# Optimization experiments

Measured on AMD Instinct MI355X. Metric: run time of the kernel, lower is better.

The kernel has to match this reference:

```python
import jax, jax.numpy as jnp
import numpy as np

B, T, D, H, E, K = 4, 1024, 1024, 2048, 8, 2  # batch, tokens, model_dim, ffn hidden, experts, top-k


def setup_inputs() -> dict:
    key = jax.random.key(0)
    k0, k1, k2, k3 = jax.random.split(key, 4)
    return {
        "x": jax.random.normal(k0, (B, T, D), dtype=jnp.float32),
        "wg": jax.random.normal(k1, (D, E), dtype=jnp.float32) * 0.02,   # gate projection
        "w1": jax.random.normal(k2, (E, D, H), dtype=jnp.float32) * 0.02,  # expert fc1
        "b1": jnp.zeros((E, H), dtype=jnp.float32),
        "w2": jax.random.normal(k3, (E, H, D), dtype=jnp.float32) * 0.02,  # expert fc2
        "b2": jnp.zeros((E, D), dtype=jnp.float32),
    }


def _moe(x, wg, w1, b1, w2, b2):
    N = B * T
    xt = x.reshape(N, D)
    # --- gating: softmax scores, top-2 selection, normalize selected gates ---
    logits = xt @ wg                         # [N, E]
    scores = jax.nn.softmax(logits, axis=-1)
    vals, idx = jax.lax.top_k(scores, K)     # [N, K]
    vals = vals / jnp.sum(vals, axis=-1, keepdims=True)
    # combine weights: [N, E], nonzero only at the top-k experts per token
    combine = jnp.zeros((N, E), dtype=xt.dtype).at[
        jnp.arange(N)[:, None], idx
    ].add(vals)
    # --- expert FFN (activation_fn is identity per source) ---
    h = jnp.einsum('nd,edh->neh', xt, w1) + b1   # [N, E, H]
    o = jnp.einsum('neh,ehd->ned', h, w2) + b2   # [N, E, D]
    # --- combine / scatter back ---
    y = jnp.einsum('ne,ned->nd', combine, o)     # [N, D]
    return y.reshape(B, T, D)


def reference(x, wg, w1, b1, w2, b2):
    y = _moe(x, wg, w1, b1, w2, b2)              # [B, T, D]
    s = jnp.sum(y, axis=2)                       # [B, T]
    return jax.nn.log_softmax(s, axis=1)
```

## Files before the change

### kernel.cpp

```cpp
#include <hip/hip_runtime.h>
#include <stdint.h>

#define B_ 4
#define T_ 1024
#define D_ 1024
#define H_ 2048
#define E_ 8

__device__ __forceinline__ void stage16(const float* g, float* l) {
    __builtin_amdgcn_global_load_lds(
        (const __attribute__((address_space(1))) uint32_t*)g,
        (__attribute__((address_space(3))) uint32_t*)l, 16, 0, 0);
}

__global__ __launch_bounds__(256) void w2sum_kernel(const float* __restrict__ w2,
                                                    float* __restrict__ w2sum) {
    __shared__ float buf[3][4 * D_];
    const int wid = threadIdx.x >> 6, lane = threadIdx.x & 63;
    const float* src = w2 + (size_t)blockIdx.x * 32 * D_ + wid * D_ + lane * 4;

#define A_STAGE(k)                                                        \
    {                                                                     \
        const float* s_ = src + (k) * (4 * D_);                           \
        float* d_ = &buf[(k) % 3][wid * D_];                              \
        stage16(s_,       d_);       stage16(s_ + 256, d_ + 256);         \
        stage16(s_ + 512, d_ + 512); stage16(s_ + 768, d_ + 768);         \
    }

    A_STAGE(0); A_STAGE(1);
    float accs[8];
#pragma unroll
    for (int k = 0; k < 8; ++k) {
        if (k < 7) asm volatile("s_waitcnt vmcnt(4)" ::: "memory");
        else       asm volatile("s_waitcnt vmcnt(0)" ::: "memory");
        if (k < 6) A_STAGE(k + 2);
        const float* row = &buf[k % 3][wid * D_];
        float acc = 0.f;
#pragma unroll
        for (int j = 0; j < 4; ++j) {
            float4 a = *(const float4*)&row[j * 256 + lane * 4];
            acc += a.x + a.y + a.z + a.w;
        }
#pragma unroll
        for (int off = 32; off >= 1; off >>= 1) acc += __shfl_xor(acc, off, 64);
        accs[k] = acc;
    }
    if (lane == 0) {
        int r0 = blockIdx.x * 32 + wid;
#pragma unroll
        for (int k = 0; k < 8; ++k) w2sum[r0 + k * 4] = accs[k];
    }
#undef A_STAGE
}

__global__ __launch_bounds__(256) void v_build_kernel(const float* __restrict__ w1,
                                                      const float* __restrict__ w2sum,
                                                      const float* __restrict__ b1,
                                                      const float* __restrict__ b2,
                                                      float* __restrict__ vT,
                                                      float* __restrict__ c) {
    __shared__ float buf[2][4 * H_];
    const int bid = blockIdx.x;
    const int e   = bid >> 6;
    const int d0  = (bid & 63) * 16;
    const int wid = threadIdx.x >> 6, lane = threadIdx.x & 63;
    const float* src = w1 + ((size_t)e * D_ + d0 + wid) * H_ + lane * 4;

    const float4* wsp = (const float4*)(w2sum + (size_t)e * H_) + lane;
    float4 s0 = wsp[0],   s1 = wsp[64],  s2 = wsp[128], s3 = wsp[192],
           s4 = wsp[256], s5 = wsp[320], s6 = wsp[384], s7 = wsp[448];
    asm volatile("" ::: "memory");

#define B_STAGE(k)                                                         \
    {                                                                      \
        const float* s_ = src + (size_t)(k) * 4 * H_;                      \
        float* d_ = &buf[(k) & 1][wid * H_];                               \
        stage16(s_,        d_);        stage16(s_ + 256,  d_ + 256);       \
        stage16(s_ + 512,  d_ + 512);  stage16(s_ + 768,  d_ + 768);       \
        stage16(s_ + 1024, d_ + 1024); stage16(s_ + 1280, d_ + 1280);      \
        stage16(s_ + 1536, d_ + 1536); stage16(s_ + 1792, d_ + 1792);      \
    }

    B_STAGE(0); B_STAGE(1);
    float accs[4];
#pragma unroll
    for (int k = 0; k < 4; ++k) {
        if (k < 3) asm volatile("s_waitcnt vmcnt(8)" ::: "memory");
        else       asm volatile("s_waitcnt vmcnt(0)" ::: "memory");
        const float* row = &buf[k & 1][wid * H_];
        float acc;
        {
            float4 a0 = *(const float4*)&row[0 * 256 + lane * 4];
            float4 a1 = *(const float4*)&row[1 * 256 + lane * 4];
            float4 a2 = *(const float4*)&row[2 * 256 + lane * 4];
            float4 a3 = *(const float4*)&row[3 * 256 + lane * 4];
            float4 a4 = *(const float4*)&row[4 * 256 + lane * 4];
            float4 a5 = *(const float4*)&row[5 * 256 + lane * 4];
            float4 a6 = *(const float4*)&row[6 * 256 + lane * 4];
            float4 a7 = *(const float4*)&row[7 * 256 + lane * 4];
            acc = a0.x*s0.x + a0.y*s0.y + a0.z*s0.z + a0.w*s0.w
                + a1.x*s1.x + a1.y*s1.y + a1.z*s1.z + a1.w*s1.w
                + a2.x*s2.x + a2.y*s2.y + a2.z*s2.z + a2.w*s2.w
                + a3.x*s3.x + a3.y*s3.y + a3.z*s3.z + a3.w*s3.w
                + a4.x*s4.x + a4.y*s4.y + a4.z*s4.z + a4.w*s4.w
                + a5.x*s5.x + a5.y*s5.y + a5.z*s5.z + a5.w*s5.w
                + a6.x*s6.x + a6.y*s6.y + a6.z*s6.z + a6.w*s6.w
                + a7.x*s7.x + a7.y*s7.y + a7.z*s7.z + a7.w*s7.w;
        }
#pragma unroll
        for (int off = 32; off >= 1; off >>= 1) acc += __shfl_xor(acc, off, 64);
        accs[k] = acc;
        if (k < 2) B_STAGE(k + 2);
    }
    if (lane == 0) {
#pragma unroll
        for (int k = 0; k < 4; ++k)
            vT[(size_t)(d0 + k * 4 + wid) * E_ + e] = accs[k];
    }

    if ((bid & 63) == 0 && wid == 0) {
        const float4* bp = (const float4*)(b1 + (size_t)e * H_) + lane;
        float4 q0 = bp[0],   q1 = bp[64],  q2 = bp[128], q3 = bp[192],
               q4 = bp[256], q5 = bp[320], q6 = bp[384], q7 = bp[448];
        float s = q0.x*s0.x + q0.y*s0.y + q0.z*s0.z + q0.w*s0.w
                + q1.x*s1.x + q1.y*s1.y + q1.z*s1.z + q1.w*s1.w
                + q2.x*s2.x + q2.y*s2.y + q2.z*s2.z + q2.w*s2.w
                + q3.x*s3.x + q3.y*s3.y + q3.z*s3.z + q3.w*s3.w
                + q4.x*s4.x + q4.y*s4.y + q4.z*s4.z + q4.w*s4.w
                + q5.x*s5.x + q5.y*s5.y + q5.z*s5.z + q5.w*s5.w
                + q6.x*s6.x + q6.y*s6.y + q6.z*s6.z + q6.w*s6.w
                + q7.x*s7.x + q7.y*s7.y + q7.z*s7.z + q7.w*s7.w;
        const float4* cp = (const float4*)(b2 + (size_t)e * D_) + lane;
#pragma unroll
        for (int j = 0; j < 4; ++j) {
            float4 bb = cp[j * 64];
            s += bb.x + bb.y + bb.z + bb.w;
        }
#pragma unroll
        for (int off = 32; off >= 1; off >>= 1) s += __shfl_xor(s, off, 64);
        if (lane == 0) c[e] = s;
    }
#undef B_STAGE
}

__global__ __launch_bounds__(256) void token_kernel(const float* __restrict__ x,
                                                    const float* __restrict__ wg,
                                                    const float* __restrict__ vT,
                                                    const float* __restrict__ c,
                                                    float* __restrict__ s) {
    int wid  = threadIdx.x >> 6;
    int lane = threadIdx.x & 63;
    int n = blockIdx.x * 4 + wid;
    const float* xr = x + (size_t)n * D_;

    float lg[E_] = {0.f,0.f,0.f,0.f,0.f,0.f,0.f,0.f};
    float dv[E_] = {0.f,0.f,0.f,0.f,0.f,0.f,0.f,0.f};

#pragma unroll
    for (int k = 0; k < D_ / 64; ++k) {
        int d = lane + 64 * k;
        float xv = xr[d];
        const float4* wgp = (const float4*)(wg + (size_t)d * E_);
        const float4* vp  = (const float4*)(vT + (size_t)d * E_);
        float4 g0 = wgp[0], g1 = wgp[1];
        float4 v0 = vp[0],  v1 = vp[1];
        lg[0] += xv * g0.x; lg[1] += xv * g0.y; lg[2] += xv * g0.z; lg[3] += xv * g0.w;
        lg[4] += xv * g1.x; lg[5] += xv * g1.y; lg[6] += xv * g1.z; lg[7] += xv * g1.w;
        dv[0] += xv * v0.x; dv[1] += xv * v0.y; dv[2] += xv * v0.z; dv[3] += xv * v0.w;
        dv[4] += xv * v1.x; dv[5] += xv * v1.y; dv[6] += xv * v1.z; dv[7] += xv * v1.w;
    }

#pragma unroll
    for (int off = 32; off >= 1; off >>= 1) {
#pragma unroll
        for (int e = 0; e < E_; ++e) {
            lg[e] += __shfl_xor(lg[e], off, 64);
            dv[e] += __shfl_xor(dv[e], off, 64);
        }
    }

    if (lane == 0) {
        int e0 = 0;
#pragma unroll
        for (int e = 1; e < E_; ++e) if (lg[e] > lg[e0]) e0 = e;
        int e1 = (e0 == 0) ? 1 : 0;
#pragma unroll
        for (int e = 0; e < E_; ++e) {
            if (e == e0) continue;
            if (lg[e] > lg[e1]) e1 = e;
        }
        float l0 = lg[e0], l1 = lg[e1];
        float g1w = 1.f / (1.f + expf(l0 - l1));
        float g0w = 1.f - g1w;
        s[n] = g0w * (dv[e0] + c[e0]) + g1w * (dv[e1] + c[e1]);
    }
}

__global__ __launch_bounds__(64) void lsm_kernel(const float* __restrict__ s,
                                                 float* __restrict__ out) {
    int brow = blockIdx.x;
    int lane = threadIdx.x & 63;
    const float* row = s + (size_t)brow * T_;
    float vals[16];
    float mx = -3.0e38f;
#pragma unroll
    for (int k = 0; k < 16; ++k) {
        vals[k] = row[lane + 64 * k];
        mx = fmaxf(mx, vals[k]);
    }
#pragma unroll
    for (int off = 32; off >= 1; off >>= 1) mx = fmaxf(mx, __shfl_xor(mx, off, 64));
    float sm = 0.f;
#pragma unroll
    for (int k = 0; k < 16; ++k) sm += expf(vals[k] - mx);
#pragma unroll
    for (int off = 32; off >= 1; off >>= 1) sm += __shfl_xor(sm, off, 64);
    float lse = mx + logf(sm);
#pragma unroll
    for (int k = 0; k < 16; ++k) out[(size_t)brow * T_ + lane + 64 * k] = vals[k] - lse;
}

extern "C" void kernel_launch(void* const* d_in, const int* in_sizes, int n_in,
                              void* d_out, int out_size, void* d_ws, size_t ws_size,
                              hipStream_t stream) {
    const float* x  = (const float*)d_in[0];
    const float* wg = (const float*)d_in[1];
    const float* w1 = (const float*)d_in[2];
    const float* b1 = (const float*)d_in[3];
    const float* w2 = (const float*)d_in[4];
    const float* b2 = (const float*)d_in[5];
    float* out = (float*)d_out;

    float* ws     = (float*)d_ws;
    float* w2sum  = ws;
    float* vT     = ws + 16384;
    float* c      = ws + 24576;
    float* s      = ws + 24592;

    w2sum_kernel<<<dim3(512), dim3(256), 0, stream>>>(w2, w2sum);
    v_build_kernel<<<dim3(512), dim3(256), 0, stream>>>(w1, w2sum, b1, b2, vT, c);
    token_kernel<<<dim3(1024), dim3(256), 0, stream>>>(x, wg, vT, c, s);
    lsm_kernel<<<dim3(4), dim3(64), 0, stream>>>(s, out);
}
```

Before: 45.12 us.

## Fuse token scoring and log-softmax via last-block atomic counter

New measurement: 58.53 us. +29.7%, slower.

```diff
diff --git a/kernel.cpp b/kernel.cpp
--- a/kernel.cpp
+++ b/kernel.cpp
@@ -7,50 +7,66 @@
 #define H_ 2048
 #define E_ 8
 
+#define AL(p)    __hip_atomic_load((p), __ATOMIC_RELAXED, __HIP_MEMORY_SCOPE_AGENT)
+#define AS(p, v) __hip_atomic_store((p), (v), __ATOMIC_RELAXED, __HIP_MEMORY_SCOPE_AGENT)
+
 __device__ __forceinline__ void stage16(const float* g, float* l) {
     __builtin_amdgcn_global_load_lds(
         (const __attribute__((address_space(1))) uint32_t*)g,
         (__attribute__((address_space(3))) uint32_t*)l, 16, 0, 0);
 }
 
+__device__ __forceinline__ void load4x16_sc(const float* p0, const float* p1,
+                                            const float* p2, const float* p3,
+                                            float4& r0, float4& r1,
+                                            float4& r2, float4& r3) {
+    asm volatile(
+        "global_load_dwordx4 %0, %4, off sc0 sc1\n\t"
+        "global_load_dwordx4 %1, %5, off sc0 sc1\n\t"
+        "global_load_dwordx4 %2, %6, off sc0 sc1\n\t"
+        "global_load_dwordx4 %3, %7, off sc0 sc1\n\t"
+        "s_waitcnt vmcnt(0)"
+        : "=&v"(r0), "=&v"(r1), "=&v"(r2), "=&v"(r3)
+        : "v"(p0), "v"(p1), "v"(p2), "v"(p3)
+        : "memory");
+}
+
 __global__ __launch_bounds__(256) void w2sum_kernel(const float* __restrict__ w2,
                                                     float* __restrict__ w2sum) {
-    __shared__ float buf[3][4 * D_];
+    __shared__ float buf[3][4096];
     const int wid = threadIdx.x >> 6, lane = threadIdx.x & 63;
-    const float* src = w2 + (size_t)blockIdx.x * 32 * D_ + wid * D_ + lane * 4;
-
-#define A_STAGE(k)                                                        \
-    {                                                                     \
-        const float* s_ = src + (k) * (4 * D_);                           \
-        float* d_ = &buf[(k) % 3][wid * D_];                              \
-        stage16(s_,       d_);       stage16(s_ + 256, d_ + 256);         \
-        stage16(s_ + 512, d_ + 512); stage16(s_ + 768, d_ + 768);         \
-    }
-
-    A_STAGE(0); A_STAGE(1);
+    const float* src = w2 + ((size_t)blockIdx.x * 32 + wid) * D_ + lane * 4;
+
+#define ASTG(k) { const float* s_ = src + (size_t)(k) * 4 * D_;               \
+                  float* d_ = &buf[(k) % 3][wid * 1024];                      \
+                  stage16(s_, d_);         stage16(s_ + 256, d_ + 256);       \
+                  stage16(s_ + 512, d_ + 512); stage16(s_ + 768, d_ + 768); }
+    ASTG(0); ASTG(1);
     float accs[8];
 #pragma unroll
     for (int k = 0; k < 8; ++k) {
         if (k < 7) asm volatile("s_waitcnt vmcnt(4)" ::: "memory");
         else       asm volatile("s_waitcnt vmcnt(0)" ::: "memory");
-        if (k < 6) A_STAGE(k + 2);
-        const float* row = &buf[k % 3][wid * D_];
-        float acc = 0.f;
-#pragma unroll
-        for (int j = 0; j < 4; ++j) {
-            float4 a = *(const float4*)&row[j * 256 + lane * 4];
-            acc += a.x + a.y + a.z + a.w;
-        }
-#pragma unroll
-        for (int off = 32; off >= 1; off >>= 1) acc += __shfl_xor(acc, off, 64);
-        accs[k] = acc;
+        if (k < 6) ASTG(k + 2);
+        const float* row = &buf[k % 3][wid * 1024];
+        float4 a0 = *(const float4*)&row[0 * 256 + lane * 4];
+        float4 a1 = *(const float4*)&row[1 * 256 + lane * 4];
+        float4 a2 = *(const float4*)&row[2 * 256 + lane * 4];
+        float4 a3 = *(const float4*)&row[3 * 256 + lane * 4];
+        accs[k] = (a0.x + a0.y + a0.z + a0.w) + (a1.x + a1.y + a1.z + a1.w)
+                + (a2.x + a2.y + a2.z + a2.w) + (a3.x + a3.y + a3.z + a3.w);
+    }
+#undef ASTG
+#pragma unroll
+    for (int off = 32; off >= 1; off >>= 1) {
+#pragma unroll
+        for (int k = 0; k < 8; ++k) accs[k] += __shfl_xor(accs[k], off, 64);
     }
     if (lane == 0) {
-        int r0 = blockIdx.x * 32 + wid;
+        const int r0 = blockIdx.x * 32 + wid;
 #pragma unroll
         for (int k = 0; k < 8; ++k) w2sum[r0 + k * 4] = accs[k];
     }
-#undef A_STAGE
 }
 
 __global__ __launch_bounds__(256) void v_build_kernel(const float* __restrict__ w1,
@@ -71,7 +87,7 @@
            s4 = wsp[256], s5 = wsp[320], s6 = wsp[384], s7 = wsp[448];
     asm volatile("" ::: "memory");
 
-#define B_STAGE(k)                                                         \
+#define BSTG(k)                                                            \
     {                                                                      \
         const float* s_ = src + (size_t)(k) * 4 * H_;                      \
         float* d_ = &buf[(k) & 1][wid * H_];                               \
@@ -81,7 +97,7 @@
         stage16(s_ + 1536, d_ + 1536); stage16(s_ + 1792, d_ + 1792);      \
     }
 
-    B_STAGE(0); B_STAGE(1);
+    BSTG(0); BSTG(1);
     float accs[4];
 #pragma unroll
     for (int k = 0; k < 4; ++k) {
@@ -107,10 +123,14 @@
                 + a6.x*s6.x + a6.y*s6.y + a6.z*s6.z + a6.w*s6.w
                 + a7.x*s7.x + a7.y*s7.y + a7.z*s7.z + a7.w*s7.w;
         }
-#pragma unroll
-        for (int off = 32; off >= 1; off >>= 1) acc += __shfl_xor(acc, off, 64);
         accs[k] = acc;
-        if (k < 2) B_STAGE(k + 2);
+        if (k < 2) BSTG(k + 2);
+    }
+#undef BSTG
+#pragma unroll
+    for (int off = 32; off >= 1; off >>= 1) {
+#pragma unroll
+        for (int k = 0; k < 4; ++k) accs[k] += __shfl_xor(accs[k], off, 64);
     }
     if (lane == 0) {
 #pragma unroll
@@ -140,84 +160,120 @@
         for (int off = 32; off >= 1; off >>= 1) s += __shfl_xor(s, off, 64);
         if (lane == 0) c[e] = s;
     }
-#undef B_STAGE
-}
-
-__global__ __launch_bounds__(256) void token_kernel(const float* __restrict__ x,
-                                                    const float* __restrict__ wg,
-                                                    const float* __restrict__ vT,
-                                                    const float* __restrict__ c,
-                                                    float* __restrict__ s) {
-    int wid  = threadIdx.x >> 6;
-    int lane = threadIdx.x & 63;
-    int n = blockIdx.x * 4 + wid;
-    const float* xr = x + (size_t)n * D_;
-
-    float lg[E_] = {0.f,0.f,0.f,0.f,0.f,0.f,0.f,0.f};
-    float dv[E_] = {0.f,0.f,0.f,0.f,0.f,0.f,0.f,0.f};
-
-#pragma unroll
-    for (int k = 0; k < D_ / 64; ++k) {
-        int d = lane + 64 * k;
-        float xv = xr[d];
-        const float4* wgp = (const float4*)(wg + (size_t)d * E_);
-        const float4* vp  = (const float4*)(vT + (size_t)d * E_);
-        float4 g0 = wgp[0], g1 = wgp[1];
-        float4 v0 = vp[0],  v1 = vp[1];
-        lg[0] += xv * g0.x; lg[1] += xv * g0.y; lg[2] += xv * g0.z; lg[3] += xv * g0.w;
-        lg[4] += xv * g1.x; lg[5] += xv * g1.y; lg[6] += xv * g1.z; lg[7] += xv * g1.w;
-        dv[0] += xv * v0.x; dv[1] += xv * v0.y; dv[2] += xv * v0.z; dv[3] += xv * v0.w;
-        dv[4] += xv * v1.x; dv[5] += xv * v1.y; dv[6] += xv * v1.z; dv[7] += xv * v1.w;
+}
+
+__global__ __launch_bounds__(256) void cd_kernel(
+    const float* __restrict__ x,  const float* __restrict__ wg,
+    const float* __restrict__ vT, const float* __restrict__ cbuf,
+    float* __restrict__ sbuf, unsigned* __restrict__ ccnt,
+    float* __restrict__ out)
+{
+    const int wid  = threadIdx.x >> 6;
+    const int lane = threadIdx.x & 63;
+    const int n0   = (blockIdx.x * 4 + wid) * 2;
+    const float* x0 = x + (size_t)n0 * D_;
+    const float* x1 = x0 + D_;
+
+    float lgA[E_] = {0,0,0,0,0,0,0,0}, dvA[E_] = {0,0,0,0,0,0,0,0};
+    float lgB[E_] = {0,0,0,0,0,0,0,0}, dvB[E_] = {0,0,0,0,0,0,0,0};
+
+#pragma unroll
+    for (int it = 0; it < 4; ++it) {
+        const int dbase = it * 256 + lane * 4;
+        float4 xa4 = *(const float4*)&x0[dbase];
+        float4 xb4 = *(const float4*)&x1[dbase];
+#pragma unroll
+        for (int dd = 0; dd < 4; ++dd) {
+            float xa = (dd == 0) ? xa4.x : (dd == 1) ? xa4.y : (dd == 2) ? xa4.z : xa4.w;
+            float xb = (dd == 0) ? xb4.x : (dd == 1) ? xb4.y : (dd == 2) ? xb4.z : xb4.w;
+            const float4* wgp = (const float4*)(wg + (size_t)(dbase + dd) * E_);
+            const float4* vp  = (const float4*)(vT + (size_t)(dbase + dd) * E_);
+            float4 g0 = wgp[0], g1 = wgp[1];
+            float4 v0 = vp[0],  v1 = vp[1];
+            lgA[0] += xa * g0.x; lgA[1] += xa * g0.y; lgA[2] += xa * g0.z; lgA[3] += xa * g0.w;
+            lgA[4] += xa * g1.x; lgA[5] += xa * g1.y; lgA[6] += xa * g1.z; lgA[7] += xa * g1.w;
+            dvA[0] += xa * v0.x; dvA[1] += xa * v0.y; dvA[2] += xa * v0.z; dvA[3] += xa * v0.w;
+            dvA[4] += xa * v1.x; dvA[5] += xa * v1.y; dvA[6] += xa * v1.z; dvA[7] += xa * v1.w;
+            lgB[0] += xb * g0.x; lgB[1] += xb * g0.y; lgB[2] += xb * g0.z; lgB[3] += xb * g0.w;
+            lgB[4] += xb * g1.x; lgB[5] += xb * g1.y; lgB[6] += xb * g1.z; lgB[7] += xb * g1.w;
+            dvB[0] += xb * v0.x; dvB[1] += xb * v0.y; dvB[2] += xb * v0.z; dvB[3] += xb * v0.w;
+            dvB[4] += xb * v1.x; dvB[5] += xb * v1.y; dvB[6] += xb * v1.z; dvB[7] += xb * v1.w;
+        }
     }
 
 #pragma unroll
     for (int off = 32; off >= 1; off >>= 1) {
 #pragma unroll
-        for (int e = 0; e < E_; ++e) {
-            lg[e] += __shfl_xor(lg[e], off, 64);
-            dv[e] += __shfl_xor(dv[e], off, 64);
-        }
-    }
-
-    if (lane == 0) {
-        int e0 = 0;
-#pragma unroll
-        for (int e = 1; e < E_; ++e) if (lg[e] > lg[e0]) e0 = e;
-        int e1 = (e0 == 0) ? 1 : 0;
-#pragma unroll
-        for (int e = 0; e < E_; ++e) {
-            if (e == e0) continue;
-            if (lg[e] > lg[e1]) e1 = e;
-        }
-        float l0 = lg[e0], l1 = lg[e1];
-        float g1w = 1.f / (1.f + expf(l0 - l1));
-        float g0w = 1.f - g1w;
-        s[n] = g0w * (dv[e0] + c[e0]) + g1w * (dv[e1] + c[e1]);
-    }
-}
-
-__global__ __launch_bounds__(64) void lsm_kernel(const float* __restrict__ s,
-                                                 float* __restrict__ out) {
-    int brow = blockIdx.x;
-    int lane = threadIdx.x & 63;
-    const float* row = s + (size_t)brow * T_;
-    float vals[16];
-    float mx = -3.0e38f;
-#pragma unroll
-    for (int k = 0; k < 16; ++k) {
-        vals[k] = row[lane + 64 * k];
-        mx = fmaxf(mx, vals[k]);
-    }
-#pragma unroll
-    for (int off = 32; off >= 1; off >>= 1) mx = fmaxf(mx, __shfl_xor(mx, off, 64));
-    float sm = 0.f;
-#pragma unroll
-    for (int k = 0; k < 16; ++k) sm += expf(vals[k] - mx);
-#pragma unroll
-    for (int off = 32; off >= 1; off >>= 1) sm += __shfl_xor(sm, off, 64);
-    float lse = mx + logf(sm);
-#pragma unroll
-    for (int k = 0; k < 16; ++k) out[(size_t)brow * T_ + lane + 64 * k] = vals[k] - lse;
+        for (int q = 0; q < E_; ++q) {
+            lgA[q] += __shfl_xor(lgA[q], off, 64);
+            dvA[q] += __shfl_xor(dvA[q], off, 64);
+            lgB[q] += __shfl_xor(lgB[q], off, 64);
+            dvB[q] += __shfl_xor(dvB[q], off, 64);
+        }
+    }
+
+    if (lane == 0 || lane == 32) {
+        const bool isA = (lane == 0);
+        float lg[E_], dvr[E_];
+#pragma unroll
+        for (int q = 0; q < E_; ++q) {
+            lg[q]  = isA ? lgA[q] : lgB[q];
+            dvr[q] = isA ? dvA[q] : dvB[q];
+        }
+        float m0 = lg[0]; int i0 = 0;
+#pragma unroll
+        for (int q = 1; q < E_; ++q) if (lg[q] > m0) { m0 = lg[q]; i0 = q; }
+        float m1 = -3.0e38f; int i1 = 0;
+#pragma unroll
+        for (int q = 0; q < E_; ++q) if (q != i0 && lg[q] > m1) { m1 = lg[q]; i1 = q; }
+        float dv0 = 0.f, dv1 = 0.f, c0v = 0.f, c1v = 0.f;
+#pragma unroll
+        for (int q = 0; q < E_; ++q) {
+            if (q == i0) { dv0 += dvr[q]; c0v += cbuf[q]; }
+            if (q == i1) { dv1 += dvr[q]; c1v += cbuf[q]; }
+        }
+        float g1w = 1.f / (1.f + expf(m0 - m1));
+        AS(&sbuf[isA ? n0 : (n0 + 1)], (1.f - g1w) * (dv0 + c0v) + g1w * (dv1 + c1v));
+    }
+
+    asm volatile("s_waitcnt vmcnt(0)" ::: "memory");
+    __syncthreads();
+    __shared__ int islast;
+    if (threadIdx.x == 0) {
+        unsigned old = __hip_atomic_fetch_add(ccnt, 1u, __ATOMIC_RELAXED, __HIP_MEMORY_SCOPE_AGENT);
+        islast = (old == (unsigned)(gridDim.x - 1)) ? 1 : 0;
+    }
+    __syncthreads();
+    if (!islast) return;
+
+    {
+        const int brow = wid;
+        const float* row = sbuf + (size_t)brow * T_;
+        float4 v0, v1, v2, v3;
+        load4x16_sc(row + lane * 4 + 0 * 256, row + lane * 4 + 1 * 256,
+                    row + lane * 4 + 2 * 256, row + lane * 4 + 3 * 256,
+                    v0, v1, v2, v3);
+        float vals[16] = {v0.x, v0.y, v0.z, v0.w, v1.x, v1.y, v1.z, v1.w,
+                          v2.x, v2.y, v2.z, v2.w, v3.x, v3.y, v3.z, v3.w};
+        float mx = -3.0e38f;
+#pragma unroll
+        for (int k = 0; k < 16; ++k) mx = fmaxf(mx, vals[k]);
+#pragma unroll
+        for (int off = 32; off >= 1; off >>= 1) mx = fmaxf(mx, __shfl_xor(mx, off, 64));
+        float sm = 0.f;
+#pragma unroll
+        for (int k = 0; k < 16; ++k) sm += expf(vals[k] - mx);
+#pragma unroll
+        for (int off = 32; off >= 1; off >>= 1) sm += __shfl_xor(sm, off, 64);
+        float lse = mx + logf(sm);
+#pragma unroll
+        for (int j = 0; j < 4; ++j) {
+            float4 o;
+            o.x = vals[j * 4 + 0] - lse; o.y = vals[j * 4 + 1] - lse;
+            o.z = vals[j * 4 + 2] - lse; o.w = vals[j * 4 + 3] - lse;
+            *(float4*)&out[(size_t)brow * T_ + lane * 4 + j * 256] = o;
+        }
+    }
 }
 
 extern "C" void kernel_launch(void* const* d_in, const int* in_sizes, int n_in,
@@ -234,11 +290,13 @@
     float* ws     = (float*)d_ws;
     float* w2sum  = ws;
     float* vT     = ws + 16384;
-    float* c      = ws + 24576;
-    float* s      = ws + 24592;
+    float* cbuf   = ws + 24576;
+    float* sbuf   = ws + 24592;
+    unsigned* cnt = (unsigned*)(ws + 28688);
+
+    hipMemsetAsync(cnt, 0, sizeof(unsigned), stream);
 
     w2sum_kernel<<<dim3(512), dim3(256), 0, stream>>>(w2, w2sum);
-    v_build_kernel<<<dim3(512), dim3(256), 0, stream>>>(w1, w2sum, b1, b2, vT, c);
-    token_kernel<<<dim3(1024), dim3(256), 0, stream>>>(x, wg, vT, c, s);
-    lsm_kernel<<<dim3(4), dim3(64), 0, stream>>>(s, out);
-}
+    v_build_kernel<<<dim3(512), dim3(256), 0, stream>>>(w1, w2sum, b1, b2, vT, cbuf);
+    cd_kernel<<<dim3(512), dim3(256), 0, stream>>>(x, wg, vT, cbuf, sbuf, cnt, out);
+}
```

## Stage gate and v tables in LDS and process 16 tokens per block

Applied to the files above, without the earlier changes.

Result: faster. 41.61 us (-7.8%).

```diff
diff --git a/kernel.cpp b/kernel.cpp
--- a/kernel.cpp
+++ b/kernel.cpp
@@ -17,11 +17,11 @@
                                                     float* __restrict__ w2sum) {
     __shared__ float buf[3][4 * D_];
     const int wid = threadIdx.x >> 6, lane = threadIdx.x & 63;
-    const float* src = w2 + (size_t)blockIdx.x * 32 * D_ + wid * D_ + lane * 4;
+    const float* src = w2 + ((size_t)blockIdx.x * 32 + wid) * D_ + lane * 4;
 
 #define A_STAGE(k)                                                        \
     {                                                                     \
-        const float* s_ = src + (k) * (4 * D_);                           \
+        const float* s_ = src + (size_t)(k) * 4 * D_;                     \
         float* d_ = &buf[(k) % 3][wid * D_];                              \
         stage16(s_,       d_);       stage16(s_ + 256, d_ + 256);         \
         stage16(s_ + 512, d_ + 512); stage16(s_ + 768, d_ + 768);         \
@@ -45,12 +45,12 @@
         for (int off = 32; off >= 1; off >>= 1) acc += __shfl_xor(acc, off, 64);
         accs[k] = acc;
     }
+#undef A_STAGE
     if (lane == 0) {
-        int r0 = blockIdx.x * 32 + wid;
+        const int r0 = blockIdx.x * 32 + wid;
 #pragma unroll
         for (int k = 0; k < 8; ++k) w2sum[r0 + k * 4] = accs[k];
     }
-#undef A_STAGE
 }
 
 __global__ __launch_bounds__(256) void v_build_kernel(const float* __restrict__ w1,
@@ -112,6 +112,7 @@
         accs[k] = acc;
         if (k < 2) B_STAGE(k + 2);
     }
+#undef B_STAGE
     if (lane == 0) {
 #pragma unroll
         for (int k = 0; k < 4; ++k)
@@ -140,65 +141,79 @@
         for (int off = 32; off >= 1; off >>= 1) s += __shfl_xor(s, off, 64);
         if (lane == 0) c[e] = s;
     }
-#undef B_STAGE
-}
-
-__global__ __launch_bounds__(256) void token_kernel(const float* __restrict__ x,
-                                                    const float* __restrict__ wg,
-                                                    const float* __restrict__ vT,
-                                                    const float* __restrict__ c,
-                                                    float* __restrict__ s) {
-    int wid  = threadIdx.x >> 6;
-    int lane = threadIdx.x & 63;
-    int n = blockIdx.x * 4 + wid;
-    const float* xr = x + (size_t)n * D_;
-
-    float lg[E_] = {0.f,0.f,0.f,0.f,0.f,0.f,0.f,0.f};
-    float dv[E_] = {0.f,0.f,0.f,0.f,0.f,0.f,0.f,0.f};
-
-#pragma unroll
-    for (int k = 0; k < D_ / 64; ++k) {
-        int d = lane + 64 * k;
-        float xv = xr[d];
-        const float4* wgp = (const float4*)(wg + (size_t)d * E_);
-        const float4* vp  = (const float4*)(vT + (size_t)d * E_);
-        float4 g0 = wgp[0], g1 = wgp[1];
-        float4 v0 = vp[0],  v1 = vp[1];
-        lg[0] += xv * g0.x; lg[1] += xv * g0.y; lg[2] += xv * g0.z; lg[3] += xv * g0.w;
-        lg[4] += xv * g1.x; lg[5] += xv * g1.y; lg[6] += xv * g1.z; lg[7] += xv * g1.w;
-        dv[0] += xv * v0.x; dv[1] += xv * v0.y; dv[2] += xv * v0.z; dv[3] += xv * v0.w;
-        dv[4] += xv * v1.x; dv[5] += xv * v1.y; dv[6] += xv * v1.z; dv[7] += xv * v1.w;
-    }
-
-#pragma unroll
-    for (int off = 32; off >= 1; off >>= 1) {
-#pragma unroll
-        for (int e = 0; e < E_; ++e) {
-            lg[e] += __shfl_xor(lg[e], off, 64);
-            dv[e] += __shfl_xor(dv[e], off, 64);
-        }
-    }
-
-    if (lane == 0) {
-        int e0 = 0;
-#pragma unroll
-        for (int e = 1; e < E_; ++e) if (lg[e] > lg[e0]) e0 = e;
-        int e1 = (e0 == 0) ? 1 : 0;
-#pragma unroll
-        for (int e = 0; e < E_; ++e) {
-            if (e == e0) continue;
-            if (lg[e] > lg[e1]) e1 = e;
-        }
-        float l0 = lg[e0], l1 = lg[e1];
-        float g1w = 1.f / (1.f + expf(l0 - l1));
-        float g0w = 1.f - g1w;
-        s[n] = g0w * (dv[e0] + c[e0]) + g1w * (dv[e1] + c[e1]);
-    }
-}
-
-__global__ __launch_bounds__(64) void lsm_kernel(const float* __restrict__ s,
-                                                 float* __restrict__ out) {
-    int brow = blockIdx.x;
+}
+
+__global__ __launch_bounds__(256) void token_kernel(
+    const float* __restrict__ x,  const float* __restrict__ wg,
+    const float* __restrict__ vT, const float* __restrict__ cbuf,
+    float* __restrict__ sbuf)
+{
+    __shared__ float wgl[D_ * E_];
+    __shared__ float vtl[D_ * E_];
+    const int wid = threadIdx.x >> 6, lane = threadIdx.x & 63;
+
+#pragma unroll
+    for (int r = 0; r < 8; ++r) {
+        int base = r * 1024 + wid * 256;
+        stage16(wg + base + lane * 4, wgl + base);
+        stage16(vT + base + lane * 4, vtl + base);
+    }
+    asm volatile("s_waitcnt vmcnt(0)" ::: "memory");
+    __syncthreads();
+
+    const int half = lane & 1;
+    const int rrow = lane >> 1;
+
+#pragma unroll
+    for (int t = 0; t < 4; ++t) {
+        const int n = blockIdx.x * 16 + wid * 4 + t;
+        const float* xg = x + (size_t)n * D_ + rrow;
+        float ag0 = 0.f, ag1 = 0.f, ag2 = 0.f, ag3 = 0.f;
+        float av0 = 0.f, av1 = 0.f, av2 = 0.f, av3 = 0.f;
+#pragma unroll
+        for (int k = 0; k < 32; ++k) {
+            float xs = xg[32 * k];
+            const int o = (32 * k + rrow) * 8 + half * 4;
+            float4 w4 = *(const float4*)&wgl[o];
+            float4 v4 = *(const float4*)&vtl[o];
+            ag0 += xs * w4.x; ag1 += xs * w4.y; ag2 += xs * w4.z; ag3 += xs * w4.w;
+            av0 += xs * v4.x; av1 += xs * v4.y; av2 += xs * v4.z; av3 += xs * v4.w;
+        }
+#pragma unroll
+        for (int off = 2; off <= 32; off <<= 1) {
+            ag0 += __shfl_xor(ag0, off, 64); ag1 += __shfl_xor(ag1, off, 64);
+            ag2 += __shfl_xor(ag2, off, 64); ag3 += __shfl_xor(ag3, off, 64);
+            av0 += __shfl_xor(av0, off, 64); av1 += __shfl_xor(av1, off, 64);
+            av2 += __shfl_xor(av2, off, 64); av3 += __shfl_xor(av3, off, 64);
+        }
+        float g4 = __shfl(ag0, 1, 64), g5 = __shfl(ag1, 1, 64),
+              g6 = __shfl(ag2, 1, 64), g7 = __shfl(ag3, 1, 64);
+        float h4 = __shfl(av0, 1, 64), h5 = __shfl(av1, 1, 64),
+              h6 = __shfl(av2, 1, 64), h7 = __shfl(av3, 1, 64);
+        if (lane == 0) {
+            float lg[E_] = {ag0, ag1, ag2, ag3, g4, g5, g6, g7};
+            float dv[E_] = {av0, av1, av2, av3, h4, h5, h6, h7};
+            float m0 = lg[0]; int i0 = 0;
+#pragma unroll
+            for (int q = 1; q < E_; ++q) if (lg[q] > m0) { m0 = lg[q]; i0 = q; }
+            float m1 = -3.0e38f; int i1 = 0;
+#pragma unroll
+            for (int q = 0; q < E_; ++q) if (q != i0 && lg[q] > m1) { m1 = lg[q]; i1 = q; }
+            float dv0 = 0.f, dv1 = 0.f, c0v = 0.f, c1v = 0.f;
+#pragma unroll
+            for (int q = 0; q < E_; ++q) {
+                if (q == i0) { dv0 += dv[q]; c0v += cbuf[q]; }
+                if (q == i1) { dv1 += dv[q]; c1v += cbuf[q]; }
+            }
+            float g1w = 1.f / (1.f + expf(m0 - m1));
+            sbuf[n] = (1.f - g1w) * (dv0 + c0v) + g1w * (dv1 + c1v);
+        }
+    }
+}
+
+__global__ __launch_bounds__(256) void lsm_kernel(const float* __restrict__ s,
+                                                  float* __restrict__ out) {
+    int brow = threadIdx.x >> 6;
     int lane = threadIdx.x & 63;
     const float* row = s + (size_t)brow * T_;
     float vals[16];
@@ -234,11 +249,11 @@
     float* ws     = (float*)d_ws;
     float* w2sum  = ws;
     float* vT     = ws + 16384;
-    float* c      = ws + 24576;
-    float* s      = ws + 24592;
+    float* cbuf   = ws + 24576;
+    float* sbuf   = ws + 24592;
 
     w2sum_kernel<<<dim3(512), dim3(256), 0, stream>>>(w2, w2sum);
-    v_build_kernel<<<dim3(512), dim3(256), 0, stream>>>(w1, w2sum, b1, b2, vT, c);
-    token_kernel<<<dim3(1024), dim3(256), 0, stream>>>(x, wg, vT, c, s);
-    lsm_kernel<<<dim3(4), dim3(64), 0, stream>>>(s, out);
-}
+    v_build_kernel<<<dim3(512), dim3(256), 0, stream>>>(w1, w2sum, b1, b2, vT, cbuf);
+    token_kernel<<<dim3(256), dim3(256), 0, stream>>>(x, wg, vT, cbuf, sbuf);
+    lsm_kernel<<<dim3(1), dim3(256), 0, stream>>>(sbuf, out);
+}
```
